# Kernel optimization log

Measured on AMD Instinct MI355X. Metric: run time of the kernel, lower is better.

The kernel has to match this reference:

```python
import jax, jax.numpy as jnp
import numpy as np

INPUT_DIM = 1024
OUTPUT_DIM = 1024
DOWN = INPUT_DIM // 8  # reduction_factor=8
NUM_TOKENS = 2


def setup_inputs() -> dict:
    key = jax.random.key(0)
    k1, k2, k3, k4, k5 = jax.random.split(key, 5)
    B, Sx, Sy = 32, 2048, 512
    x = jax.random.normal(k1, (B, Sx, INPUT_DIM), dtype=jnp.float32)
    y = jax.random.normal(k2, (B, Sy, INPUT_DIM), dtype=jnp.float32)
    # nn.Parameter(torch.rand(...)) -> uniform [0,1)
    latent_tokens = jax.random.uniform(k3, (NUM_TOKENS, INPUT_DIM), dtype=jnp.float32)
    gate = jnp.zeros((1,), dtype=jnp.float32)
    # Conv1d kernel_size=1, no bias == pointwise matmul; kaiming-uniform-ish init
    lim_d = 1.0 / np.sqrt(INPUT_DIM)
    lim_u = 1.0 / np.sqrt(DOWN)
    W_down = jax.random.uniform(k4, (DOWN, INPUT_DIM), dtype=jnp.float32, minval=-lim_d, maxval=lim_d)
    W_up = jax.random.uniform(k5, (OUTPUT_DIM, DOWN), dtype=jnp.float32, minval=-lim_u, maxval=lim_u)
    return {"x": x, "y": y, "latent_tokens": latent_tokens, "gate": gate,
            "W_down": W_down, "W_up": W_up}


def reference(x, y, latent_tokens, gate, W_down, W_up):
    # tokens attend over y:  [B,T,Sy] softmax over Sy
    att_y2t = jax.nn.softmax(jnp.einsum('td,bsd->bts', latent_tokens, y), axis=-1)
    tokens = latent_tokens[None] + jnp.einsum('bts,bsd->btd', att_y2t, y)  # [B,T,D]
    # x attends over tokens: [B,Sx,T] softmax over T
    att_t2x = jax.nn.softmax(jnp.einsum('bsd,btd->bst', x, tokens), axis=-1)
    x_res = jnp.einsum('bst,btd->bsd', att_t2x, tokens)
    x = x + gate * x_res
    # 1x1 conv bottleneck: down -> ReLU -> up (pointwise matmuls)
    z = jax.nn.relu(jnp.einsum('bsd,ed->bse', x, W_down))
    out = jnp.einsum('bse,oe->bso', z, W_up)
    return out
```

## Files before the change

### kernel.cpp

```cpp
#include <hip/hip_runtime.h>
#include <hip/hip_bf16.h>

#define B_N 32
#define SX 2048
#define SY 512
#define DIM 1024
#define NTOK 2
#define DN 128
#define ODIM 1024
#define BM 64
#define BK 64
#define NT 16
#define RING 3

typedef __bf16 bf16;
typedef __bf16 bf16x8 __attribute__((ext_vector_type(8)));
typedef __bf16 bf16x4 __attribute__((ext_vector_type(4)));
typedef float f32x4 __attribute__((ext_vector_type(4)));

typedef __attribute__((address_space(3))) unsigned char lds_u8;
typedef const __attribute__((address_space(1))) unsigned char glb_u8;

__device__ __forceinline__ f32x4 mfma16(bf16x8 a, bf16x8 b, f32x4 c) {
  return __builtin_amdgcn_mfma_f32_16x16x32_bf16(a, b, c, 0, 0, 0);
}
__device__ __forceinline__ void gll16(const void* g, void* l) {
  __builtin_amdgcn_global_load_lds((glb_u8*)g, (lds_u8*)l, 16, 0, 0);
}

__global__ __launch_bounds__(256) void prep_kernel(const float* __restrict__ Wd,
                                                   const float* __restrict__ Wu,
                                                   bf16* __restrict__ wdb,
                                                   bf16* __restrict__ wub) {
  int i = blockIdx.x * 256 + threadIdx.x;
  if (i < DN * DIM) {
    wdb[i] = (bf16)Wd[i];
    wub[i] = (bf16)Wu[i];
  }
}

__global__ __launch_bounds__(256) void tokens_kernel(const float* __restrict__ y,
                                                     const float* __restrict__ lat,
                                                     const float* __restrict__ gate,
                                                     float* __restrict__ tokens) {
  if (gate[0] == 0.0f) return;
  __shared__ float s_lat[NTOK][DIM];
  __shared__ float s_sc[NTOK][SY];
  int b = blockIdx.x;
  int tid = threadIdx.x, wave = tid >> 6, lane = tid & 63;
  const float* yb = y + (size_t)b * SY * DIM;
  for (int i = tid; i < NTOK * DIM; i += 256) ((float*)s_lat)[i] = lat[i];
  __syncthreads();
  for (int s = wave * 128; s < wave * 128 + 128; ++s) {
    const float* yr = yb + (size_t)s * DIM;
    float d0 = 0.f, d1 = 0.f;
#pragma unroll
    for (int i = 0; i < 4; ++i) {
      f32x4 v = *(const f32x4*)(yr + lane * 4 + i * 256);
      f32x4 l0 = *(const f32x4*)(&s_lat[0][lane * 4 + i * 256]);
      f32x4 l1 = *(const f32x4*)(&s_lat[1][lane * 4 + i * 256]);
      d0 += v[0] * l0[0] + v[1] * l0[1] + v[2] * l0[2] + v[3] * l0[3];
      d1 += v[0] * l1[0] + v[1] * l1[1] + v[2] * l1[2] + v[3] * l1[3];
    }
#pragma unroll
    for (int off = 32; off > 0; off >>= 1) {
      d0 += __shfl_xor(d0, off);
      d1 += __shfl_xor(d1, off);
    }
    if (lane == 0) { s_sc[0][s] = d0; s_sc[1][s] = d1; }
  }
  __syncthreads();
  if (wave < 2) {
    float m = -3.4e38f;
    for (int s = lane; s < SY; s += 64) m = fmaxf(m, s_sc[wave][s]);
#pragma unroll
    for (int off = 32; off > 0; off >>= 1) m = fmaxf(m, __shfl_xor(m, off));
    float sum = 0.f;
    for (int s = lane; s < SY; s += 64) {
      float e = expf(s_sc[wave][s] - m);
      s_sc[wave][s] = e;
      sum += e;
    }
#pragma unroll
    for (int off = 32; off > 0; off >>= 1) sum += __shfl_xor(sum, off);
    float inv = 1.f / sum;
    for (int s = lane; s < SY; s += 64) s_sc[wave][s] *= inv;
  }
  __syncthreads();
  float a0[4] = {0.f, 0.f, 0.f, 0.f}, a1[4] = {0.f, 0.f, 0.f, 0.f};
  for (int s = 0; s < SY; ++s) {
    float p0 = s_sc[0][s], p1 = s_sc[1][s];
    const float* yr = yb + (size_t)s * DIM;
#pragma unroll
    for (int i = 0; i < 4; ++i) {
      float v = yr[tid + i * 256];
      a0[i] += p0 * v;
      a1[i] += p1 * v;
    }
  }
  float* tb = tokens + (size_t)b * NTOK * DIM;
#pragma unroll
  for (int i = 0; i < 4; ++i) {
    tb[tid + i * 256] = s_lat[0][tid + i * 256] + a0[i];
    tb[DIM + tid + i * 256] = s_lat[1][tid + i * 256] + a1[i];
  }
}

__global__ __launch_bounds__(256) void xprime_kernel(const float* __restrict__ x,
                                                     const float* __restrict__ gate,
                                                     const float* __restrict__ tokens,
                                                     float* __restrict__ xp) {
  float g = gate[0];
  if (g == 0.0f) return;
  __shared__ float s_tok[NTOK][DIM];
  __shared__ float s_c[BM][2];
  int tid = threadIdx.x, w = tid >> 6, lane = tid & 63;
  size_t m0 = (size_t)blockIdx.x * BM;
  int b = (int)(m0 / SX);
  const float* xb = x + m0 * DIM;
  const float* tokb = tokens + (size_t)b * NTOK * DIM;
  for (int i = tid; i < NTOK * DIM; i += 256) ((float*)s_tok)[i] = tokb[i];
  __syncthreads();
  for (int i = 0; i < 16; ++i) {
    int r = w * 16 + i;
    const float* xrow = xb + (size_t)r * DIM;
    float d0 = 0.f, d1 = 0.f;
#pragma unroll
    for (int c = 0; c < 4; ++c) {
      f32x4 v = *(const f32x4*)(xrow + lane * 4 + c * 256);
      f32x4 t0 = *(const f32x4*)(&s_tok[0][lane * 4 + c * 256]);
      f32x4 t1 = *(const f32x4*)(&s_tok[1][lane * 4 + c * 256]);
      d0 += v[0] * t0[0] + v[1] * t0[1] + v[2] * t0[2] + v[3] * t0[3];
      d1 += v[0] * t1[0] + v[1] * t1[1] + v[2] * t1[2] + v[3] * t1[3];
    }
#pragma unroll
    for (int off = 32; off > 0; off >>= 1) {
      d0 += __shfl_xor(d0, off);
      d1 += __shfl_xor(d1, off);
    }
    if (lane == 0) {
      float mm = fmaxf(d0, d1);
      float e0 = expf(d0 - mm), e1 = expf(d1 - mm);
      float inv = g / (e0 + e1);
      s_c[r][0] = e0 * inv;
      s_c[r][1] = e1 * inv;
    }
  }
  __syncthreads();
  float* xpb = xp + m0 * DIM;
  for (int r = w * 16; r < w * 16 + 16; ++r) {
    float c0 = s_c[r][0], c1 = s_c[r][1];
#pragma unroll
    for (int c = 0; c < 4; ++c) {
      f32x4 v = *(const f32x4*)(xb + (size_t)r * DIM + lane * 4 + c * 256);
      f32x4 t0 = *(const f32x4*)(&s_tok[0][lane * 4 + c * 256]);
      f32x4 t1 = *(const f32x4*)(&s_tok[1][lane * 4 + c * 256]);
      f32x4 o;
#pragma unroll
      for (int j = 0; j < 4; ++j) o[j] = v[j] + c0 * t0[j] + c1 * t1[j];
      *(f32x4*)(xpb + (size_t)r * DIM + lane * 4 + c * 256) = o;
    }
  }
}

__global__ __launch_bounds__(512) void main_kernel(const float* __restrict__ x,
                                                   const float* __restrict__ gate,
                                                   const float* __restrict__ xp,
                                                   const bf16* __restrict__ wdb,
                                                   const bf16* __restrict__ wub,
                                                   float* __restrict__ out) {
  __shared__ __align__(16) char smem[114688];

  int tid = threadIdx.x, w = tid >> 6, l = tid & 63;
  int lq = l >> 4, lr = l & 15;
  size_t m0 = (size_t)blockIdx.x * BM;
  float g = gate[0];
  const float* xb = ((g != 0.f) ? xp : x) + m0 * DIM;

  const char* xsrc[2];
  const char* wsrc[2];
#pragma unroll
  for (int j = 0; j < 2; ++j) {
    int xr = w * 8 + j * 4 + (l >> 4);
    int xcb = ((l & 15) * 16) ^ ((j * 4 + (l >> 4)) << 5);
    xsrc[j] = (const char*)xb + (size_t)xr * (DIM * 4) + xcb;
    int wr_ = w * 16 + j * 8 + (l >> 3);
    int wcb = ((l & 7) * 16) ^ ((l >> 3) << 4);
    wsrc[j] = (const char*)wdb + (size_t)wr_ * (DIM * 2) + wcb;
  }

  f32x4 acc[4] = {};

  auto STAGE = [&](int t) {
    int b = t % RING;
#pragma unroll
    for (int j = 0; j < 2; ++j)
      gll16(xsrc[j] + (size_t)t * (BK * 4),
            smem + b * 16384 + (w * 8 + j * 4) * 256);
#pragma unroll
    for (int j = 0; j < 2; ++j)
      gll16(wsrc[j] + (size_t)t * (BK * 2),
            smem + 49152 + b * 16384 + (w * 16 + j * 8) * 128);
  };

  auto COMP = [&](int b) {
    const char* xt = smem + b * 16384;
    const char* wt = smem + 49152 + b * 16384;
#pragma unroll
    for (int kc = 0; kc < 2; ++kc) {
      int dn = w * 16 + lr;
      bf16x8 wdf = *(const bf16x8*)(wt + dn * 128 +
                                    ((kc * 64 + lq * 16) ^ ((lr & 7) << 4)));
#pragma unroll
      for (int mt = 0; mt < 4; ++mt) {
        int row = mt * 16 + lr;
        int sz = (row & 7) << 5;
        int kb = kc * 128 + lq * 32;
        f32x4 a0 = *(const f32x4*)(xt + row * 256 + (kb ^ sz));
        f32x4 a1 = *(const f32x4*)(xt + row * 256 + ((kb + 16) ^ sz));
        bf16x8 xf;
#pragma unroll
        for (int jj = 0; jj < 4; ++jj) {
          xf[jj] = (bf16)a0[jj];
          xf[4 + jj] = (bf16)a1[jj];
        }
        acc[mt] = mfma16(wdf, xf, acc[mt]);
      }
    }
  };

  STAGE(0);
  STAGE(1);
  STAGE(2);

#pragma unroll
  for (int t = 0; t < NT; ++t) {
    if (t > 0 && t + 2 < NT) STAGE(t + 2);
    if (t + 2 < NT) {
      asm volatile("s_waitcnt vmcnt(8)" ::: "memory");
    } else if (t == NT - 2) {
      asm volatile("s_waitcnt vmcnt(4)" ::: "memory");
    } else {
      asm volatile("s_waitcnt vmcnt(0)" ::: "memory");
    }
    __builtin_amdgcn_sched_barrier(0);
    __builtin_amdgcn_s_barrier();
    COMP(t % RING);
    __builtin_amdgcn_sched_barrier(0);
    __builtin_amdgcn_s_barrier();
  }

  char* zls = smem + 98304;
#pragma unroll
  for (int mt = 0; mt < 4; ++mt) {
    int xr = mt * 16 + lr;
    int dn = w * 16 + lq * 4;
    bf16x4 pk;
#pragma unroll
    for (int r = 0; r < 4; ++r) pk[r] = (bf16)fmaxf(acc[mt][r], 0.f);
    *(bf16x4*)(zls + xr * (DN * 2) + ((dn * 2) ^ ((xr & 7) << 4))) = pk;
  }
  __syncthreads();

  bf16x8 zF[4][4];
#pragma unroll
  for (int mt = 0; mt < 4; ++mt)
#pragma unroll
    for (int kt = 0; kt < 4; ++kt) {
      int xr = mt * 16 + lr;
      zF[kt][mt] = *(const bf16x8*)(zls + xr * (DN * 2) +
                                    (((kt * 32 + lq * 8) * 2) ^ ((xr & 7) << 4)));
    }

  float* ob = out + m0 * ODIM;
#pragma unroll 2
  for (int oc16 = 0; oc16 < 8; ++oc16) {
    int base = w * 128 + oc16 * 16;
    bf16x8 wu[4];
#pragma unroll
    for (int kt = 0; kt < 4; ++kt)
      wu[kt] = *(const bf16x8*)(wub + (size_t)(base + lr) * DN + kt * 32 + lq * 8);
    f32x4 a2[4] = {};
#pragma unroll
    for (int kt = 0; kt < 4; ++kt)
#pragma unroll
      for (int mt = 0; mt < 4; ++mt)
        a2[mt] = mfma16(wu[kt], zF[kt][mt], a2[mt]);
#pragma unroll
    for (int mt = 0; mt < 4; ++mt)
      *(f32x4*)(ob + (size_t)(mt * 16 + lr) * ODIM + base + lq * 4) = a2[mt];
  }
}

extern "C" void kernel_launch(void* const* d_in, const int* in_sizes, int n_in,
                              void* d_out, int out_size, void* d_ws, size_t ws_size,
                              hipStream_t stream) {
  const float* x = (const float*)d_in[0];
  const float* y = (const float*)d_in[1];
  const float* lat = (const float*)d_in[2];
  const float* gate = (const float*)d_in[3];
  const float* Wd = (const float*)d_in[4];
  const float* Wu = (const float*)d_in[5];
  float* out = (float*)d_out;
  char* ws = (char*)d_ws;

  float* tokens = (float*)ws;
  bf16* wdb = (bf16*)(ws + 262144);
  bf16* wub = (bf16*)(ws + 524288);

  prep_kernel<<<(DN * DIM + 255) / 256, 256, 0, stream>>>(Wd, Wu, wdb, wub);
  tokens_kernel<<<B_N, 256, 0, stream>>>(y, lat, gate, tokens);
  xprime_kernel<<<(B_N * SX) / BM, 256, 0, stream>>>(x, gate, tokens, out);
  main_kernel<<<(B_N * SX) / BM, 512, 0, stream>>>(x, gate, out, wdb, wub, out);
}
```

Before: 146.0 us.

## Deepen load ring to four stages and retile down-proj warps as 2x4

Raises the LDS ring buffer from three to four stages, prefetching one more K-tile ahead and issuing the next stage after the post-compute barrier. It also changes the per-warp tile of the down-projection from 64 rows by 16 channels to 32 rows by 32 channels. This halves the per-warp fp32-to-bf16 conversions of x and reuses each converted fragment across two MFMAs. Compute is wrapped in s_setprio. LDS use grows to 144 KB, which could limit occupancy to one block per CU.

```diff
diff --git a/kernel.cpp b/kernel.cpp
--- a/kernel.cpp
+++ b/kernel.cpp
@@ -11,7 +11,7 @@
 #define BM 64
 #define BK 64
 #define NT 16
-#define RING 3
+#define RING 4
 
 typedef __bf16 bf16;
 typedef __bf16 bf16x8 __attribute__((ext_vector_type(8)));
@@ -169,10 +169,11 @@
                                                    const bf16* __restrict__ wdb,
                                                    const bf16* __restrict__ wub,
                                                    float* __restrict__ out) {
-  __shared__ __align__(16) char smem[114688];
+  __shared__ __align__(16) char smem[147456];
 
   int tid = threadIdx.x, w = tid >> 6, l = tid & 63;
   int lq = l >> 4, lr = l & 15;
+  int wr = w >> 2, wc = w & 3;
   size_t m0 = (size_t)blockIdx.x * BM;
   float g = gate[0];
   const float* xb = ((g != 0.f) ? xp : x) + m0 * DIM;
@@ -189,10 +190,10 @@
     wsrc[j] = (const char*)wdb + (size_t)wr_ * (DIM * 2) + wcb;
   }
 
-  f32x4 acc[4] = {};
+  f32x4 acc[2][2] = {};
 
   auto STAGE = [&](int t) {
-    int b = t % RING;
+    int b = t & 3;
 #pragma unroll
     for (int j = 0; j < 2; ++j)
       gll16(xsrc[j] + (size_t)t * (BK * 4),
@@ -200,20 +201,25 @@
 #pragma unroll
     for (int j = 0; j < 2; ++j)
       gll16(wsrc[j] + (size_t)t * (BK * 2),
-            smem + 49152 + b * 16384 + (w * 16 + j * 8) * 128);
+            smem + 65536 + b * 16384 + (w * 16 + j * 8) * 128);
   };
 
   auto COMP = [&](int b) {
     const char* xt = smem + b * 16384;
-    const char* wt = smem + 49152 + b * 16384;
+    const char* wt = smem + 65536 + b * 16384;
+    __builtin_amdgcn_s_setprio(1);
 #pragma unroll
     for (int kc = 0; kc < 2; ++kc) {
-      int dn = w * 16 + lr;
-      bf16x8 wdf = *(const bf16x8*)(wt + dn * 128 +
-                                    ((kc * 64 + lq * 16) ^ ((lr & 7) << 4)));
-#pragma unroll
-      for (int mt = 0; mt < 4; ++mt) {
-        int row = mt * 16 + lr;
+      bf16x8 wdf[2];
+#pragma unroll
+      for (int nf = 0; nf < 2; ++nf) {
+        int dn = wc * 32 + nf * 16 + lr;
+        wdf[nf] = *(const bf16x8*)(wt + dn * 128 +
+                                   ((kc * 64 + lq * 16) ^ ((lr & 7) << 4)));
+      }
+#pragma unroll
+      for (int mt = 0; mt < 2; ++mt) {
+        int row = wr * 32 + mt * 16 + lr;
         int sz = (row & 7) << 5;
         int kb = kc * 128 + lq * 32;
         f32x4 a0 = *(const f32x4*)(xt + row * 256 + (kb ^ sz));
@@ -224,19 +230,23 @@
           xf[jj] = (bf16)a0[jj];
           xf[4 + jj] = (bf16)a1[jj];
         }
-        acc[mt] = mfma16(wdf, xf, acc[mt]);
+        acc[mt][0] = mfma16(wdf[0], xf, acc[mt][0]);
+        acc[mt][1] = mfma16(wdf[1], xf, acc[mt][1]);
       }
     }
+    __builtin_amdgcn_s_setprio(0);
   };
 
   STAGE(0);
   STAGE(1);
   STAGE(2);
+  STAGE(3);
 
 #pragma unroll
   for (int t = 0; t < NT; ++t) {
-    if (t > 0 && t + 2 < NT) STAGE(t + 2);
-    if (t + 2 < NT) {
+    if (t <= NT - 4) {
+      asm volatile("s_waitcnt vmcnt(12)" ::: "memory");
+    } else if (t == NT - 3) {
       asm volatile("s_waitcnt vmcnt(8)" ::: "memory");
     } else if (t == NT - 2) {
       asm volatile("s_waitcnt vmcnt(4)" ::: "memory");
@@ -245,21 +255,24 @@
     }
     __builtin_amdgcn_sched_barrier(0);
     __builtin_amdgcn_s_barrier();
-    COMP(t % RING);
+    COMP(t & 3);
     __builtin_amdgcn_sched_barrier(0);
     __builtin_amdgcn_s_barrier();
-  }
-
-  char* zls = smem + 98304;
-#pragma unroll
-  for (int mt = 0; mt < 4; ++mt) {
-    int xr = mt * 16 + lr;
-    int dn = w * 16 + lq * 4;
-    bf16x4 pk;
-#pragma unroll
-    for (int r = 0; r < 4; ++r) pk[r] = (bf16)fmaxf(acc[mt][r], 0.f);
-    *(bf16x4*)(zls + xr * (DN * 2) + ((dn * 2) ^ ((xr & 7) << 4))) = pk;
-  }
+    if (t + 4 < NT) STAGE(t + 4);
+  }
+
+  char* zls = smem + 131072;
+#pragma unroll
+  for (int mt = 0; mt < 2; ++mt)
+#pragma unroll
+    for (int nf = 0; nf < 2; ++nf) {
+      int xr = wr * 32 + mt * 16 + lr;
+      int dn = wc * 32 + nf * 16 + lq * 4;
+      bf16x4 pk;
+#pragma unroll
+      for (int r = 0; r < 4; ++r) pk[r] = (bf16)fmaxf(acc[mt][nf][r], 0.f);
+      *(bf16x4*)(zls + xr * (DN * 2) + ((dn * 2) ^ ((xr & 7) << 4))) = pk;
+    }
   __syncthreads();
 
   bf16x8 zF[4][4];
```

New measurement: 144.8 us, median of 3. Within noise of the previous version (-0.9%).
